# Kernel tuning notes

Hardware: AMD Instinct MI355X
Metric: run time of the kernel (lower is better)

Reference implementation:

```python
import jax, jax.numpy as jnp
import numpy as np

MAX_H = 64
MAX_W = 64

def setup_inputs() -> dict:
    key = jax.random.key(0)
    ks = jax.random.split(key, 6)
    in_f, out_f = 128, 128
    x0 = jax.random.normal(ks[0], (32, 64, 64, in_f), dtype=jnp.float32)
    x1 = jax.random.normal(ks[1], (32, 32, 64, in_f), dtype=jnp.float32)
    x2 = jax.random.normal(ks[2], (32, 64, 32, in_f), dtype=jnp.float32)
    x3 = jax.random.normal(ks[3], (32, 32, 32, in_f), dtype=jnp.float32)
    stdv = 1.0 / np.sqrt(in_f)
    weight = jax.random.uniform(ks[4], (out_f, in_f), minval=-stdv, maxval=stdv, dtype=jnp.float32)
    bias = jax.random.uniform(ks[5], (out_f,), minval=-stdv, maxval=stdv, dtype=jnp.float32)
    return {"x0": x0, "x1": x1, "x2": x2, "x3": x3, "weight": weight, "bias": bias}

def reference(x0, x1, x2, x3, weight, bias):
    # Grouped/ragged linear: flatten each variable-shaped tensor to rows of
    # in_features, concatenate, apply shared y = x @ W^T + b, then reshape to
    # (-1, max_H, max_W, out_features) as in the original CUDA path.
    k = weight.shape[0]
    flat = jnp.concatenate([x.reshape(-1, x.shape[-1]) for x in (x0, x1, x2, x3)], axis=0)
    out = flat @ weight.T + bias  # [total_rows, out_features]
    return out.reshape(-1, MAX_H, MAX_W, k)
```

## Files before the change

kernel.cpp:

```cpp
#include <hip/hip_runtime.h>
#include <hip/hip_bf16.h>


typedef __attribute__((ext_vector_type(8))) short bf8_t;
typedef __attribute__((ext_vector_type(4))) float f4_t;

__device__ __forceinline__ unsigned short f2bf(float f) {
    unsigned u = __builtin_bit_cast(unsigned, f);
    u += 0x7fffu + ((u >> 16) & 1u);
    return (unsigned short)(u >> 16);
}

#define SEG0 131072L
#define SEG1 196608L
#define SEG2 262144L

__global__ __launch_bounds__(256)
void lin_kernel(const float* __restrict__ x0, const float* __restrict__ x1,
                const float* __restrict__ x2, const float* __restrict__ x3,
                const float* __restrict__ W, const float* __restrict__ bias,
                float* __restrict__ out)
{
    __shared__ unsigned short Wl[128 * 128];
    __shared__ float bl[128];

    const int tid = threadIdx.x;

#pragma unroll
    for (int i = 0; i < 16; ++i) {
        int f  = i * 256 + tid;
        int n  = f >> 5;
        int k4 = f & 31;
        f4_t v = reinterpret_cast<const f4_t*>(W)[f];
        unsigned long long p =
              (unsigned long long)f2bf(v.x)
            | ((unsigned long long)f2bf(v.y) << 16)
            | ((unsigned long long)f2bf(v.z) << 32)
            | ((unsigned long long)f2bf(v.w) << 48);
        int sc = (k4 >> 1) ^ (n & 7);
        *reinterpret_cast<unsigned long long*>(&Wl[n * 128 + sc * 8 + (k4 & 1) * 4]) = p;
    }
    if (tid < 128) bl[tid] = bias[tid];
    __syncthreads();

    const int wave = tid >> 6;
    const int lane = tid & 63;
    const int lm   = lane & 15;
    const int lk   = lane >> 4;
    const int nsw  = lm & 7;

    const long blk0 = (long)blockIdx.x * 128;
    const float* xp; long loc;
    if      (blk0 < SEG0) { xp = x0; loc = blk0; }
    else if (blk0 < SEG1) { xp = x1; loc = blk0 - SEG0; }
    else if (blk0 < SEG2) { xp = x2; loc = blk0 - SEG1; }
    else                  { xp = x3; loc = blk0 - SEG2; }

    for (int it = 0; it < 2; ++it) {
        const long r  = (long)it * 64 + wave * 16 + lm;
        const float* xr = xp + (loc + r) * 128;

        f4_t raw[8];
#pragma unroll
        for (int ks = 0; ks < 4; ++ks) {
            const float* p = xr + ks * 32 + lk * 8;
            raw[2 * ks]     = *reinterpret_cast<const f4_t*>(p);
            raw[2 * ks + 1] = *reinterpret_cast<const f4_t*>(p + 4);
        }
        bf8_t xf[4];
#pragma unroll
        for (int ks = 0; ks < 4; ++ks) {
            bf8_t t;
            t[0] = (short)f2bf(raw[2 * ks].x);
            t[1] = (short)f2bf(raw[2 * ks].y);
            t[2] = (short)f2bf(raw[2 * ks].z);
            t[3] = (short)f2bf(raw[2 * ks].w);
            t[4] = (short)f2bf(raw[2 * ks + 1].x);
            t[5] = (short)f2bf(raw[2 * ks + 1].y);
            t[6] = (short)f2bf(raw[2 * ks + 1].z);
            t[7] = (short)f2bf(raw[2 * ks + 1].w);
            xf[ks] = t;
        }

        f4_t acc[8];
#pragma unroll
        for (int nt = 0; nt < 8; ++nt)
            acc[nt] = *reinterpret_cast<const f4_t*>(&bl[nt * 16 + lk * 4]);

#pragma unroll
        for (int nt = 0; nt < 8; ++nt) {
            const int nrow = nt * 16 + lm;
#pragma unroll
            for (int ks = 0; ks < 4; ++ks) {
                const int c = (ks * 4 + lk) ^ nsw;
                bf8_t wf = *reinterpret_cast<const bf8_t*>(&Wl[nrow * 128 + c * 8]);
                acc[nt] = __builtin_amdgcn_mfma_f32_16x16x32_bf16(wf, xf[ks], acc[nt], 0, 0, 0);
            }
        }

        float* orow = out + (blk0 + r) * 128;
#pragma unroll
        for (int nt = 0; nt < 8; ++nt)
            *reinterpret_cast<f4_t*>(orow + nt * 16 + lk * 4) = acc[nt];
    }
}

extern "C" void kernel_launch(void* const* d_in, const int* in_sizes, int n_in,
                              void* d_out, int out_size, void* d_ws, size_t ws_size,
                              hipStream_t stream) {
    const float* x0 = (const float*)d_in[0];
    const float* x1 = (const float*)d_in[1];
    const float* x2 = (const float*)d_in[2];
    const float* x3 = (const float*)d_in[3];
    const float* W  = (const float*)d_in[4];
    const float* b  = (const float*)d_in[5];
    float* out = (float*)d_out;

    hipLaunchKernelGGL(lin_kernel, dim3(2304), dim3(256), 0, stream,
                       x0, x1, x2, x3, W, b, out);
}
```

Before: 66.17 us.

## Use 512-thread blocks covering 256 rows, issuing both tiles' loads before compute

Blocks grow to 8 waves covering 256 rows, so the weight conversion into shared memory is paid once per 256 rows instead of once per 128, and the grid halves. Each wave now issues the global loads for both of its 16-row tiles before any MFMA work, giving more memory-level parallelism. Activation conversion switches to the hardware __float2bfloat16 intrinsic. The cost is higher register pressure from holding two raw tiles, with launch bounds asking for 4 blocks per CU.

Result: slower. 116.5 us (+76.1%).

```diff
diff --git a/kernel.cpp b/kernel.cpp
--- a/kernel.cpp
+++ b/kernel.cpp
@@ -5,7 +5,11 @@
 typedef __attribute__((ext_vector_type(8))) short bf8_t;
 typedef __attribute__((ext_vector_type(4))) float f4_t;
 
-__device__ __forceinline__ unsigned short f2bf(float f) {
+__device__ __forceinline__ short bfc(float f) {
+    return __builtin_bit_cast(short, __float2bfloat16(f));
+}
+
+__device__ __forceinline__ unsigned short f2bf_rne(float f) {
     unsigned u = __builtin_bit_cast(unsigned, f);
     u += 0x7fffu + ((u >> 16) & 1u);
     return (unsigned short)(u >> 16);
@@ -15,7 +19,48 @@
 #define SEG1 196608L
 #define SEG2 262144L
 
-__global__ __launch_bounds__(256)
+__device__ __forceinline__ void tile_mfma_store(
+    const f4_t (&raw)[8], const unsigned short* __restrict__ Wl,
+    const float* __restrict__ bl, float* __restrict__ orow,
+    int lm, int lk, int nsw)
+{
+    bf8_t xf[4];
+#pragma unroll
+    for (int ks = 0; ks < 4; ++ks) {
+        bf8_t t;
+        t[0] = bfc(raw[2 * ks].x);
+        t[1] = bfc(raw[2 * ks].y);
+        t[2] = bfc(raw[2 * ks].z);
+        t[3] = bfc(raw[2 * ks].w);
+        t[4] = bfc(raw[2 * ks + 1].x);
+        t[5] = bfc(raw[2 * ks + 1].y);
+        t[6] = bfc(raw[2 * ks + 1].z);
+        t[7] = bfc(raw[2 * ks + 1].w);
+        xf[ks] = t;
+    }
+
+    f4_t acc[8];
+#pragma unroll
+    for (int nt = 0; nt < 8; ++nt)
+        acc[nt] = *reinterpret_cast<const f4_t*>(&bl[nt * 16 + lk * 4]);
+
+#pragma unroll
+    for (int nt = 0; nt < 8; ++nt) {
+        const int nrow = nt * 16 + lm;
+#pragma unroll
+        for (int ks = 0; ks < 4; ++ks) {
+            const int c = (ks * 4 + lk) ^ nsw;
+            bf8_t wf = *reinterpret_cast<const bf8_t*>(&Wl[nrow * 128 + c * 8]);
+            acc[nt] = __builtin_amdgcn_mfma_f32_16x16x32_bf16(wf, xf[ks], acc[nt], 0, 0, 0);
+        }
+    }
+
+#pragma unroll
+    for (int nt = 0; nt < 8; ++nt)
+        *reinterpret_cast<f4_t*>(orow + nt * 16 + lk * 4) = acc[nt];
+}
+
+__global__ __launch_bounds__(512, 4)
 void lin_kernel(const float* __restrict__ x0, const float* __restrict__ x1,
                 const float* __restrict__ x2, const float* __restrict__ x3,
                 const float* __restrict__ W, const float* __restrict__ bias,
@@ -27,16 +72,16 @@
     const int tid = threadIdx.x;
 
 #pragma unroll
-    for (int i = 0; i < 16; ++i) {
-        int f  = i * 256 + tid;
+    for (int i = 0; i < 8; ++i) {
+        int f  = i * 512 + tid;
         int n  = f >> 5;
         int k4 = f & 31;
         f4_t v = reinterpret_cast<const f4_t*>(W)[f];
         unsigned long long p =
-              (unsigned long long)f2bf(v.x)
-            | ((unsigned long long)f2bf(v.y) << 16)
-            | ((unsigned long long)f2bf(v.z) << 32)
-            | ((unsigned long long)f2bf(v.w) << 48);
+              (unsigned long long)f2bf_rne(v.x)
+            | ((unsigned long long)f2bf_rne(v.y) << 16)
+            | ((unsigned long long)f2bf_rne(v.z) << 32)
+            | ((unsigned long long)f2bf_rne(v.w) << 48);
         int sc = (k4 >> 1) ^ (n & 7);
         *reinterpret_cast<unsigned long long*>(&Wl[n * 128 + sc * 8 + (k4 & 1) * 4]) = p;
     }
@@ -49,60 +94,36 @@
     const int lk   = lane >> 4;
     const int nsw  = lm & 7;
 
-    const long blk0 = (long)blockIdx.x * 128;
+    const long base = (long)blockIdx.x * 256;
     const float* xp; long loc;
-    if      (blk0 < SEG0) { xp = x0; loc = blk0; }
-    else if (blk0 < SEG1) { xp = x1; loc = blk0 - SEG0; }
-    else if (blk0 < SEG2) { xp = x2; loc = blk0 - SEG1; }
-    else                  { xp = x3; loc = blk0 - SEG2; }
+    if      (base < SEG0) { xp = x0; loc = base; }
+    else if (base < SEG1) { xp = x1; loc = base - SEG0; }
+    else if (base < SEG2) { xp = x2; loc = base - SEG1; }
+    else                  { xp = x3; loc = base - SEG2; }
 
-    for (int it = 0; it < 2; ++it) {
-        const long r  = (long)it * 64 + wave * 16 + lm;
-        const float* xr = xp + (loc + r) * 128;
+    const int r = wave * 16 + lm;
+    const float* pA = xp + (loc + r) * 128;
+    const float* pB = pA + 128 * 128;
 
-        f4_t raw[8];
+    f4_t rawA[8], rawB[8];
 #pragma unroll
-        for (int ks = 0; ks < 4; ++ks) {
-            const float* p = xr + ks * 32 + lk * 8;
-            raw[2 * ks]     = *reinterpret_cast<const f4_t*>(p);
-            raw[2 * ks + 1] = *reinterpret_cast<const f4_t*>(p + 4);
-        }
-        bf8_t xf[4];
+    for (int ks = 0; ks < 4; ++ks) {
+        const float* p = pA + ks * 32 + lk * 8;
+        rawA[2 * ks]     = *reinterpret_cast<const f4_t*>(p);
+        rawA[2 * ks + 1] = *reinterpret_cast<const f4_t*>(p + 4);
+    }
 #pragma unroll
-        for (int ks = 0; ks < 4; ++ks) {
-            bf8_t t;
-            t[0] = (short)f2bf(raw[2 * ks].x);
-            t[1] = (short)f2bf(raw[2 * ks].y);
-            t[2] = (short)f2bf(raw[2 * ks].z);
-            t[3] = (short)f2bf(raw[2 * ks].w);
-            t[4] = (short)f2bf(raw[2 * ks + 1].x);
-            t[5] = (short)f2bf(raw[2 * ks + 1].y);
-            t[6] = (short)f2bf(raw[2 * ks + 1].z);
-            t[7] = (short)f2bf(raw[2 * ks + 1].w);
-            xf[ks] = t;
-        }
+    for (int ks = 0; ks < 4; ++ks) {
+        const float* p = pB + ks * 32 + lk * 8;
+        rawB[2 * ks]     = *reinterpret_cast<const f4_t*>(p);
+        rawB[2 * ks + 1] = *reinterpret_cast<const f4_t*>(p + 4);
+    }
 
-        f4_t acc[8];
-#pragma unroll
-        for (int nt = 0; nt < 8; ++nt)
-            acc[nt] = *reinterpret_cast<const f4_t*>(&bl[nt * 16 + lk * 4]);
+    float* oA = out + (base + r) * 128;
+    float* oB = oA + 128 * 128;
 
-#pragma unroll
-        for (int nt = 0; nt < 8; ++nt) {
-            const int nrow = nt * 16 + lm;
-#pragma unroll
-            for (int ks = 0; ks < 4; ++ks) {
-                const int c = (ks * 4 + lk) ^ nsw;
-                bf8_t wf = *reinterpret_cast<const bf8_t*>(&Wl[nrow * 128 + c * 8]);
-                acc[nt] = __builtin_amdgcn_mfma_f32_16x16x32_bf16(wf, xf[ks], acc[nt], 0, 0, 0);
-            }
-        }
-
-        float* orow = out + (blk0 + r) * 128;
-#pragma unroll
-        for (int nt = 0; nt < 8; ++nt)
-            *reinterpret_cast<f4_t*>(orow + nt * 16 + lk * 4) = acc[nt];
-    }
+    tile_mfma_store(rawA, Wl, bl, oA, lm, lk, nsw);
+    tile_mfma_store(rawB, Wl, bl, oB, lm, lk, nsw);
 }
 
 extern "C" void kernel_launch(void* const* d_in, const int* in_sizes, int n_in,
@@ -116,6 +137,6 @@
     const float* b  = (const float*)d_in[5];
     float* out = (float*)d_out;
 
-    hipLaunchKernelGGL(lin_kernel, dim3(2304), dim3(256), 0, stream,
+    hipLaunchKernelGGL(lin_kernel, dim3(1152), dim3(512), 0, stream,
                        x0, x1, x2, x3, W, b, out);
 }
```

## Persistent blocks with double-buffered async LDS staging and register-resident weights

Applied to the files above, without the earlier changes.

Switches to 512 persistent blocks that each process nine 64-row tiles. Each tile is double-buffered into swizzled LDS using global_load_lds, so the next tile's load overlaps the current tile's MFMA work. Each wave keeps its 32-column slice of W and the bias in registers, which drops the per-block staging of the full 128x128 weight matrix in LDS. Output uses nontemporal stores and the conversion uses the library bf16 cast. The trade-offs are fewer resident blocks from 64KB of LDS and a full vmcnt wait plus barrier on every tile.

After: 65.81 us. No clear change (-0.5%).

```diff
diff --git a/kernel.cpp b/kernel.cpp
--- a/kernel.cpp
+++ b/kernel.cpp
@@ -5,15 +5,79 @@
 typedef __attribute__((ext_vector_type(8))) short bf8_t;
 typedef __attribute__((ext_vector_type(4))) float f4_t;
 
-__device__ __forceinline__ unsigned short f2bf(float f) {
-    unsigned u = __builtin_bit_cast(unsigned, f);
-    u += 0x7fffu + ((u >> 16) & 1u);
-    return (unsigned short)(u >> 16);
+typedef const unsigned __attribute__((address_space(1)))* gp_t;
+typedef unsigned __attribute__((address_space(3)))* lp_t;
+
+__device__ __forceinline__ short bfc(float f) {
+    return __builtin_bit_cast(short, __float2bfloat16(f));
 }
 
 #define SEG0 131072L
 #define SEG1 196608L
 #define SEG2 262144L
+
+__device__ __forceinline__ const float* tile_src(long gr,
+    const float* __restrict__ x0, const float* __restrict__ x1,
+    const float* __restrict__ x2, const float* __restrict__ x3)
+{
+    const float* xp; long loc;
+    if      (gr < SEG0) { xp = x0; loc = gr; }
+    else if (gr < SEG1) { xp = x1; loc = gr - SEG0; }
+    else if (gr < SEG2) { xp = x2; loc = gr - SEG1; }
+    else                { xp = x3; loc = gr - SEG2; }
+    return xp + loc * 128;
+}
+
+__device__ __forceinline__ void stage_tile(const float* __restrict__ src,
+                                           float* __restrict__ buf,
+                                           int wave, int lane)
+{
+#pragma unroll
+    for (int i = 0; i < 8; ++i) {
+        const int c  = i * 256 + wave * 64 + lane;
+        const int r  = c >> 5;
+        const int kc = c & 31;
+        const float* g = src + r * 128 + ((kc ^ (r & 7)) << 2);
+        float* l = buf + (i * 256 + wave * 64) * 4;
+        __builtin_amdgcn_global_load_lds((gp_t)g, (lp_t)l, 16, 0, 0);
+    }
+}
+
+__device__ __forceinline__ void compute_tile(const float* __restrict__ buf,
+    float* __restrict__ obase, const bf8_t (&wf)[2][4],
+    f4_t bf0, f4_t bf1, int wave, int lm, int lk)
+{
+#pragma unroll
+    for (int s = 0; s < 4; ++s) {
+        const int row = s * 16 + lm;
+        const int sw  = row & 7;
+        f4_t raw[8];
+#pragma unroll
+        for (int ks = 0; ks < 4; ++ks) {
+            const int c0 = ks * 8 + lk * 2;
+            raw[2*ks]   = *reinterpret_cast<const f4_t*>(buf + row * 128 + (((c0    ) ^ sw) << 2));
+            raw[2*ks+1] = *reinterpret_cast<const f4_t*>(buf + row * 128 + (((c0 + 1) ^ sw) << 2));
+        }
+        bf8_t xf[4];
+#pragma unroll
+        for (int ks = 0; ks < 4; ++ks) {
+            f4_t a = raw[2*ks], b = raw[2*ks+1];
+            bf8_t t;
+            t[0]=bfc(a.x); t[1]=bfc(a.y); t[2]=bfc(a.z); t[3]=bfc(a.w);
+            t[4]=bfc(b.x); t[5]=bfc(b.y); t[6]=bfc(b.z); t[7]=bfc(b.w);
+            xf[ks] = t;
+        }
+        f4_t acc0 = bf0, acc1 = bf1;
+#pragma unroll
+        for (int ks = 0; ks < 4; ++ks) {
+            acc0 = __builtin_amdgcn_mfma_f32_16x16x32_bf16(wf[0][ks], xf[ks], acc0, 0, 0, 0);
+            acc1 = __builtin_amdgcn_mfma_f32_16x16x32_bf16(wf[1][ks], xf[ks], acc1, 0, 0, 0);
+        }
+        float* orow = obase + (long)row * 128 + wave * 32 + lk * 4;
+        __builtin_nontemporal_store(acc0, reinterpret_cast<f4_t*>(orow));
+        __builtin_nontemporal_store(acc1, reinterpret_cast<f4_t*>(orow + 16));
+    }
+}
 
 __global__ __launch_bounds__(256)
 void lin_kernel(const float* __restrict__ x0, const float* __restrict__ x1,
@@ -21,87 +85,52 @@
                 const float* __restrict__ W, const float* __restrict__ bias,
                 float* __restrict__ out)
 {
-    __shared__ unsigned short Wl[128 * 128];
-    __shared__ float bl[128];
+    __shared__ float xb0[64 * 128];
+    __shared__ float xb1[64 * 128];
 
-    const int tid = threadIdx.x;
-
-#pragma unroll
-    for (int i = 0; i < 16; ++i) {
-        int f  = i * 256 + tid;
-        int n  = f >> 5;
-        int k4 = f & 31;
-        f4_t v = reinterpret_cast<const f4_t*>(W)[f];
-        unsigned long long p =
-              (unsigned long long)f2bf(v.x)
-            | ((unsigned long long)f2bf(v.y) << 16)
-            | ((unsigned long long)f2bf(v.z) << 32)
-            | ((unsigned long long)f2bf(v.w) << 48);
-        int sc = (k4 >> 1) ^ (n & 7);
-        *reinterpret_cast<unsigned long long*>(&Wl[n * 128 + sc * 8 + (k4 & 1) * 4]) = p;
-    }
-    if (tid < 128) bl[tid] = bias[tid];
-    __syncthreads();
-
+    const int tid  = threadIdx.x;
     const int wave = tid >> 6;
     const int lane = tid & 63;
     const int lm   = lane & 15;
     const int lk   = lane >> 4;
-    const int nsw  = lm & 7;
 
-    const long blk0 = (long)blockIdx.x * 128;
-    const float* xp; long loc;
-    if      (blk0 < SEG0) { xp = x0; loc = blk0; }
-    else if (blk0 < SEG1) { xp = x1; loc = blk0 - SEG0; }
-    else if (blk0 < SEG2) { xp = x2; loc = blk0 - SEG1; }
-    else                  { xp = x3; loc = blk0 - SEG2; }
+    const long blk0 = (long)blockIdx.x * 576;
 
-    for (int it = 0; it < 2; ++it) {
-        const long r  = (long)it * 64 + wave * 16 + lm;
-        const float* xr = xp + (loc + r) * 128;
+    stage_tile(tile_src(blk0, x0, x1, x2, x3), xb0, wave, lane);
 
-        f4_t raw[8];
+    bf8_t wf[2][4];
+#pragma unroll
+    for (int nt = 0; nt < 2; ++nt) {
+        const int nW = wave * 32 + nt * 16 + lm;
 #pragma unroll
         for (int ks = 0; ks < 4; ++ks) {
-            const float* p = xr + ks * 32 + lk * 8;
-            raw[2 * ks]     = *reinterpret_cast<const f4_t*>(p);
-            raw[2 * ks + 1] = *reinterpret_cast<const f4_t*>(p + 4);
+            const float* p = W + nW * 128 + ks * 32 + lk * 8;
+            f4_t a = *reinterpret_cast<const f4_t*>(p);
+            f4_t b = *reinterpret_cast<const f4_t*>(p + 4);
+            bf8_t t;
+            t[0]=bfc(a.x); t[1]=bfc(a.y); t[2]=bfc(a.z); t[3]=bfc(a.w);
+            t[4]=bfc(b.x); t[5]=bfc(b.y); t[6]=bfc(b.z); t[7]=bfc(b.w);
+            wf[nt][ks] = t;
         }
-        bf8_t xf[4];
-#pragma unroll
-        for (int ks = 0; ks < 4; ++ks) {
-            bf8_t t;
-            t[0] = (short)f2bf(raw[2 * ks].x);
-            t[1] = (short)f2bf(raw[2 * ks].y);
-            t[2] = (short)f2bf(raw[2 * ks].z);
-            t[3] = (short)f2bf(raw[2 * ks].w);
-            t[4] = (short)f2bf(raw[2 * ks + 1].x);
-            t[5] = (short)f2bf(raw[2 * ks + 1].y);
-            t[6] = (short)f2bf(raw[2 * ks + 1].z);
-            t[7] = (short)f2bf(raw[2 * ks + 1].w);
-            xf[ks] = t;
+    }
+    const f4_t bf0 = *reinterpret_cast<const f4_t*>(bias + wave * 32 +      lk * 4);
+    const f4_t bf1 = *reinterpret_cast<const f4_t*>(bias + wave * 32 + 16 + lk * 4);
+
+    asm volatile("s_waitcnt vmcnt(0)" ::: "memory");
+    __builtin_amdgcn_s_barrier();
+
+    float* cur = xb0;
+    float* nxt = xb1;
+#pragma unroll 1
+    for (int t = 0; t < 9; ++t) {
+        if (t < 8)
+            stage_tile(tile_src(blk0 + (t + 1) * 64, x0, x1, x2, x3), nxt, wave, lane);
+        compute_tile(cur, out + (blk0 + t * 64) * 128, wf, bf0, bf1, wave, lm, lk);
+        if (t < 8) {
+            asm volatile("s_waitcnt vmcnt(0)" ::: "memory");
+            __builtin_amdgcn_s_barrier();
         }
-
-        f4_t acc[8];
-#pragma unroll
-        for (int nt = 0; nt < 8; ++nt)
-            acc[nt] = *reinterpret_cast<const f4_t*>(&bl[nt * 16 + lk * 4]);
-
-#pragma unroll
-        for (int nt = 0; nt < 8; ++nt) {
-            const int nrow = nt * 16 + lm;
-#pragma unroll
-            for (int ks = 0; ks < 4; ++ks) {
-                const int c = (ks * 4 + lk) ^ nsw;
-                bf8_t wf = *reinterpret_cast<const bf8_t*>(&Wl[nrow * 128 + c * 8]);
-                acc[nt] = __builtin_amdgcn_mfma_f32_16x16x32_bf16(wf, xf[ks], acc[nt], 0, 0, 0);
-            }
-        }
-
-        float* orow = out + (blk0 + r) * 128;
-#pragma unroll
-        for (int nt = 0; nt < 8; ++nt)
-            *reinterpret_cast<f4_t*>(orow + nt * 16 + lk * 4) = acc[nt];
+        float* tmp = cur; cur = nxt; nxt = tmp;
     }
 }
 
@@ -116,6 +145,6 @@
     const float* b  = (const float*)d_in[5];
     float* out = (float*)d_out;
 
-    hipLaunchKernelGGL(lin_kernel, dim3(2304), dim3(256), 0, stream,
+    hipLaunchKernelGGL(lin_kernel, dim3(512), dim3(256), 0, stream,
                        x0, x1, x2, x3, W, b, out);
 }
```

## Process 256 rows per block, fully unrolled, with shuffled bias and intrinsic bf16 conversion

Applied to the files above, without the earlier changes.

Each block now handles 256 rows instead of 128, which halves the grid and amortizes the per-block W load and bf16 conversion into LDS over twice as many rows. The row loop is fully unrolled and the segment lookup is done per row. Bias moves from shared memory into registers and is broadcast with wave shuffles. Input conversion uses the __float2bfloat16 intrinsic, and launch bounds request 5 blocks per CU. The cost is higher register pressure and fewer blocks to spread across the CUs, and the extra shuffles add instructions.

Measured after the change: 68.81 us. 1.04x slower.

```diff
diff --git a/kernel.cpp b/kernel.cpp
--- a/kernel.cpp
+++ b/kernel.cpp
@@ -5,7 +5,11 @@
 typedef __attribute__((ext_vector_type(8))) short bf8_t;
 typedef __attribute__((ext_vector_type(4))) float f4_t;
 
-__device__ __forceinline__ unsigned short f2bf(float f) {
+__device__ __forceinline__ short bfc(float f) {
+    return __builtin_bit_cast(short, __float2bfloat16(f));
+}
+
+__device__ __forceinline__ unsigned short f2bf_rne(float f) {
     unsigned u = __builtin_bit_cast(unsigned, f);
     u += 0x7fffu + ((u >> 16) & 1u);
     return (unsigned short)(u >> 16);
@@ -15,14 +19,13 @@
 #define SEG1 196608L
 #define SEG2 262144L
 
-__global__ __launch_bounds__(256)
+__global__ __launch_bounds__(256, 5)
 void lin_kernel(const float* __restrict__ x0, const float* __restrict__ x1,
                 const float* __restrict__ x2, const float* __restrict__ x3,
                 const float* __restrict__ W, const float* __restrict__ bias,
                 float* __restrict__ out)
 {
     __shared__ unsigned short Wl[128 * 128];
-    __shared__ float bl[128];
 
     const int tid = threadIdx.x;
 
@@ -33,14 +36,13 @@
         int k4 = f & 31;
         f4_t v = reinterpret_cast<const f4_t*>(W)[f];
         unsigned long long p =
-              (unsigned long long)f2bf(v.x)
-            | ((unsigned long long)f2bf(v.y) << 16)
-            | ((unsigned long long)f2bf(v.z) << 32)
-            | ((unsigned long long)f2bf(v.w) << 48);
+              (unsigned long long)f2bf_rne(v.x)
+            | ((unsigned long long)f2bf_rne(v.y) << 16)
+            | ((unsigned long long)f2bf_rne(v.z) << 32)
+            | ((unsigned long long)f2bf_rne(v.w) << 48);
         int sc = (k4 >> 1) ^ (n & 7);
         *reinterpret_cast<unsigned long long*>(&Wl[n * 128 + sc * 8 + (k4 & 1) * 4]) = p;
     }
-    if (tid < 128) bl[tid] = bias[tid];
     __syncthreads();
 
     const int wave = tid >> 6;
@@ -49,16 +51,21 @@
     const int lk   = lane >> 4;
     const int nsw  = lm & 7;
 
-    const long blk0 = (long)blockIdx.x * 128;
-    const float* xp; long loc;
-    if      (blk0 < SEG0) { xp = x0; loc = blk0; }
-    else if (blk0 < SEG1) { xp = x1; loc = blk0 - SEG0; }
-    else if (blk0 < SEG2) { xp = x2; loc = blk0 - SEG1; }
-    else                  { xp = x3; loc = blk0 - SEG2; }
+    const f4_t bb = *reinterpret_cast<const f4_t*>(bias + ((lane & 31) << 2));
 
-    for (int it = 0; it < 2; ++it) {
-        const long r  = (long)it * 64 + wave * 16 + lm;
-        const float* xr = xp + (loc + r) * 128;
+    const long r0 = (long)blockIdx.x * 256 + wave * 16 + lm;
+
+#pragma unroll
+    for (int t = 0; t < 4; ++t) {
+        const long gr = r0 + t * 64;
+
+        const float* xp; long loc;
+        if      (gr < SEG0) { xp = x0; loc = gr; }
+        else if (gr < SEG1) { xp = x1; loc = gr - SEG0; }
+        else if (gr < SEG2) { xp = x2; loc = gr - SEG1; }
+        else                { xp = x3; loc = gr - SEG2; }
+        const float* xr   = xp + loc * 128;
+        float*       orow = out + gr * 128;
 
         f4_t raw[8];
 #pragma unroll
@@ -67,25 +74,27 @@
             raw[2 * ks]     = *reinterpret_cast<const f4_t*>(p);
             raw[2 * ks + 1] = *reinterpret_cast<const f4_t*>(p + 4);
         }
+
         bf8_t xf[4];
 #pragma unroll
         for (int ks = 0; ks < 4; ++ks) {
-            bf8_t t;
-            t[0] = (short)f2bf(raw[2 * ks].x);
-            t[1] = (short)f2bf(raw[2 * ks].y);
-            t[2] = (short)f2bf(raw[2 * ks].z);
-            t[3] = (short)f2bf(raw[2 * ks].w);
-            t[4] = (short)f2bf(raw[2 * ks + 1].x);
-            t[5] = (short)f2bf(raw[2 * ks + 1].y);
-            t[6] = (short)f2bf(raw[2 * ks + 1].z);
-            t[7] = (short)f2bf(raw[2 * ks + 1].w);
-            xf[ks] = t;
+            f4_t a = raw[2 * ks], b = raw[2 * ks + 1];
+            bf8_t w;
+            w[0]=bfc(a.x); w[1]=bfc(a.y); w[2]=bfc(a.z); w[3]=bfc(a.w);
+            w[4]=bfc(b.x); w[5]=bfc(b.y); w[6]=bfc(b.z); w[7]=bfc(b.w);
+            xf[ks] = w;
         }
 
+        int z = 0;
+        asm volatile("" : "+v"(z));
+        const int lkz = lk + z;
         f4_t acc[8];
 #pragma unroll
-        for (int nt = 0; nt < 8; ++nt)
-            acc[nt] = *reinterpret_cast<const f4_t*>(&bl[nt * 16 + lk * 4]);
+        for (int nt = 0; nt < 8; ++nt) {
+#pragma unroll
+            for (int e = 0; e < 4; ++e)
+                acc[nt][e] = __shfl(bb[e], nt * 4 + lkz);
+        }
 
 #pragma unroll
         for (int nt = 0; nt < 8; ++nt) {
@@ -98,7 +107,6 @@
             }
         }
 
-        float* orow = out + (blk0 + r) * 128;
 #pragma unroll
         for (int nt = 0; nt < 8; ++nt)
             *reinterpret_cast<f4_t*>(orow + nt * 16 + lk * 4) = acc[nt];
@@ -116,6 +124,6 @@
     const float* b  = (const float*)d_in[5];
     float* out = (float*)d_out;
 
-    hipLaunchKernelGGL(lin_kernel, dim3(2304), dim3(256), 0, stream,
+    hipLaunchKernelGGL(lin_kernel, dim3(1152), dim3(256), 0, stream,
                        x0, x1, x2, x3, W, b, out);
 }
```
